# Kernel tuning notes

Hardware: AMD Instinct MI355X
Metric: run time of the kernel (lower is better)

## Reference

```python
import jax, jax.numpy as jnp
import numpy as np

V, E, H, B, T, O = 50000, 300, 512, 32, 256, 10


def setup_inputs() -> dict:
    key = jax.random.key(0)
    ks = jax.random.split(key, 12)
    sc = 1.0 / np.sqrt(H)  # torch LSTM init scale
    rn = lambda k, shape, s: (jax.random.normal(k, shape, jnp.float32) * s)
    return {
        "tokens": jax.random.randint(ks[0], (B, T), 0, V),
        "embed_table": rn(ks[1], (V, E), 0.1),
        "W_ih_f": rn(ks[2], (4 * H, E), sc),
        "W_hh_f": rn(ks[3], (4 * H, H), sc),
        "b_ih_f": rn(ks[4], (4 * H,), sc),
        "b_hh_f": rn(ks[5], (4 * H,), sc),
        "W_ih_b": rn(ks[6], (4 * H, E), sc),
        "W_hh_b": rn(ks[7], (4 * H, H), sc),
        "b_ih_b": rn(ks[8], (4 * H,), sc),
        "b_hh_b": rn(ks[9], (4 * H,), sc),
        "W_out": rn(ks[10], (O, 2 * H), 1.0 / np.sqrt(2 * H)),
        "b_out": rn(ks[11], (O,), 0.01),
    }


def _lstm_dir(x_tbe, W_ih, W_hh, b_ih, b_hh, reverse):
    """One LSTM direction. x_tbe: [T,B,E]. Returns hidden seq [T,B,H]."""
    Hd = W_hh.shape[1]
    # precompute input contribution for all timesteps: [T,B,4H]
    xg = jnp.einsum('tbe,ge->tbg', x_tbe, W_ih) + b_ih + b_hh

    def step(carry, xt):
        h, c = carry
        gates = xt + h @ W_hh.T                    # [B,4H]
        i, f, g, o = jnp.split(gates, 4, axis=-1)  # torch gate order i,f,g,o
        c = jax.nn.sigmoid(f) * c + jax.nn.sigmoid(i) * jnp.tanh(g)
        h = jax.nn.sigmoid(o) * jnp.tanh(c)
        return (h, c), h

    h0 = jnp.zeros((x_tbe.shape[1], Hd), x_tbe.dtype)
    _, hs = jax.lax.scan(step, (h0, h0), xg, reverse=reverse)
    return hs


def reference(tokens, embed_table, W_ih_f, W_hh_f, b_ih_f, b_hh_f,
              W_ih_b, W_hh_b, b_ih_b, b_hh_b, W_out, b_out):
    x = embed_table[tokens]          # [B,T,E] embedding lookup (dropout_e=0 in eval)
    x = x.transpose(1, 0, 2)         # [T,B,E] time-major, as in the torch module
    hf = _lstm_dir(x, W_ih_f, W_hh_f, b_ih_f, b_hh_f, reverse=False)
    hb = _lstm_dir(x, W_ih_b, W_hh_b, b_ih_b, b_hh_b, reverse=True)
    rnn_out = jnp.concatenate([hf, hb], axis=-1)   # [T,B,2H]
    # relu then max-pool over the full time axis (kernel = seq_len)
    pooled = jnp.max(jax.nn.relu(rnn_out), axis=0)  # [B,2H]
    logits = pooled @ W_out.T + b_out               # [B,O]
    return logits, rnn_out
```

## Files before the change

### kernel.cpp

```cpp
#include <hip/hip_runtime.h>
#include <hip/hip_bf16.h>

#define B_ 32
#define T_ 256
#define E_ 300
#define EP_ 320
#define H_ 512
#define O_ 10
#define TEAM 32
#define THR 512
#define HPB 16
#define NBLK 512

typedef __attribute__((ext_vector_type(8))) short bf16x8;
typedef __attribute__((ext_vector_type(4))) float f32x4;

__device__ __forceinline__ float bf2f(unsigned short u) {
  unsigned v = ((unsigned)u) << 16; float f; __builtin_memcpy(&f, &v, 4); return f;
}
__device__ __forceinline__ short f2bf(float x) {
  unsigned u; __builtin_memcpy(&u, &x, 4);
  unsigned r = u + 0x7fffu + ((u >> 16) & 1u);
  return (short)(r >> 16);
}

__global__ __launch_bounds__(256) void xprep_k(
    const int* __restrict__ tokens, const float* __restrict__ embed,
    unsigned short* __restrict__ xb)
{
  const int t = blockIdx.x;
  __shared__ int tok_s[B_];
  const int tid = threadIdx.x;
  if (tid < B_) tok_s[tid] = tokens[tid * T_ + t];
  __syncthreads();
  const size_t plane = (size_t)T_ * B_ * EP_;
  unsigned short* hi = xb;
  unsigned short* lo = xb + plane;
  for (int i = tid; i < B_ * E_; i += 256) {
    const int b = i / E_, e = i - b * E_;
    const float v = embed[(size_t)tok_s[b] * E_ + e];
    const short h = f2bf(v);
    const short l = f2bf(v - bf2f((unsigned short)h));
    const size_t o = ((size_t)t * B_ + b) * EP_ + e;
    hi[o] = (unsigned short)h; lo[o] = (unsigned short)l;
  }
  for (int i = tid; i < B_ * (EP_ - E_); i += 256) {
    const int b = i / (EP_ - E_), e = E_ + (i - b * (EP_ - E_));
    const size_t o = ((size_t)t * B_ + b) * EP_ + e;
    hi[o] = 0; lo[o] = 0;
  }
}

__global__ __launch_bounds__(320) void wprep_k(
    const float* __restrict__ Wf, const float* __restrict__ Wb,
    unsigned short* __restrict__ wp)
{
  const int row = blockIdx.x;
  const int dir = blockIdx.y;
  const int e   = threadIdx.x;
  const float* __restrict__ W = dir ? Wb : Wf;
  short h = 0, l = 0;
  if (e < E_) {
    const float v = W[(size_t)row * E_ + e];
    h = f2bf(v);
    l = f2bf(v - bf2f((unsigned short)h));
  }
  const size_t hiB = ((size_t)(dir * 2 + 0)) * 2048 * EP_;
  const size_t loB = ((size_t)(dir * 2 + 1)) * 2048 * EP_;
  wp[hiB + (size_t)row * EP_ + e] = (unsigned short)h;
  wp[loB + (size_t)row * EP_ + e] = (unsigned short)l;
}

__global__ __launch_bounds__(256) void xg_mfma_k(
    const unsigned short* __restrict__ wp,
    const unsigned short* __restrict__ xb,
    const float* __restrict__ bif, const float* __restrict__ bhf,
    const float* __restrict__ bib, const float* __restrict__ bhb,
    __hip_bfloat16* __restrict__ xg)
{
  const int rt  = blockIdx.x;
  const int t   = blockIdx.y;
  const int dir = blockIdx.z;
  const int tid = threadIdx.x;
  const int l = tid & 63, w = tid >> 6;
  const int m = l & 15, q = l >> 4;
  const int rowb = rt * 64 + w * 16;

  const float* __restrict__ bi = dir ? bib : bif;
  const float* __restrict__ bh = dir ? bhb : bhf;

  bf16x8 ahi[10], alo[10];
  {
    const unsigned short* whi =
        wp + ((size_t)(dir * 2 + 0) * 2048 + rowb + m) * EP_ + q * 8;
    const unsigned short* wlo =
        wp + ((size_t)(dir * 2 + 1) * 2048 + rowb + m) * EP_ + q * 8;
    #pragma unroll
    for (int kt = 0; kt < 10; ++kt) {
      ahi[kt] = *(const bf16x8*)(whi + kt * 32);
      alo[kt] = *(const bf16x8*)(wlo + kt * 32);
    }
  }

  const size_t plane = (size_t)T_ * B_ * EP_;
  const unsigned short* xh0 = xb + ((size_t)t * B_ + m     ) * EP_ + q * 8;
  const unsigned short* xh1 = xb + ((size_t)t * B_ + m + 16) * EP_ + q * 8;

  f32x4 acc0 = {0.f, 0.f, 0.f, 0.f}, acc1 = {0.f, 0.f, 0.f, 0.f};
  #pragma unroll
  for (int kt = 0; kt < 10; ++kt) {
    bf16x8 b0h = *(const bf16x8*)(xh0 + kt * 32);
    bf16x8 b0l = *(const bf16x8*)(xh0 + plane + kt * 32);
    bf16x8 b1h = *(const bf16x8*)(xh1 + kt * 32);
    bf16x8 b1l = *(const bf16x8*)(xh1 + plane + kt * 32);
    acc0 = __builtin_amdgcn_mfma_f32_16x16x32_bf16(ahi[kt], b0h, acc0, 0, 0, 0);
    acc0 = __builtin_amdgcn_mfma_f32_16x16x32_bf16(alo[kt], b0h, acc0, 0, 0, 0);
    acc0 = __builtin_amdgcn_mfma_f32_16x16x32_bf16(ahi[kt], b0l, acc0, 0, 0, 0);
    acc1 = __builtin_amdgcn_mfma_f32_16x16x32_bf16(ahi[kt], b1h, acc1, 0, 0, 0);
    acc1 = __builtin_amdgcn_mfma_f32_16x16x32_bf16(alo[kt], b1h, acc1, 0, 0, 0);
    acc1 = __builtin_amdgcn_mfma_f32_16x16x32_bf16(ahi[kt], b1l, acc1, 0, 0, 0);
  }

  const int r4 = rowb + q * 4;
  const float4 bi4 = *(const float4*)(bi + r4);
  const float4 bh4 = *(const float4*)(bh + r4);
  const float bias0 = bi4.x + bh4.x, bias1 = bi4.y + bh4.y;
  const float bias2 = bi4.z + bh4.z, bias3 = bi4.w + bh4.w;
  unsigned short* og =
      (unsigned short*)xg + ((size_t)(dir * T_ + t) * 2048 + r4) * B_;
  og[0 * B_ + m]      = (unsigned short)f2bf(acc0[0] + bias0);
  og[1 * B_ + m]      = (unsigned short)f2bf(acc0[1] + bias1);
  og[2 * B_ + m]      = (unsigned short)f2bf(acc0[2] + bias2);
  og[3 * B_ + m]      = (unsigned short)f2bf(acc0[3] + bias3);
  og[0 * B_ + m + 16] = (unsigned short)f2bf(acc1[0] + bias0);
  og[1 * B_ + m + 16] = (unsigned short)f2bf(acc1[1] + bias1);
  og[2 * B_ + m + 16] = (unsigned short)f2bf(acc1[2] + bias2);
  og[3 * B_ + m + 16] = (unsigned short)f2bf(acc1[3] + bias3);
}

__device__ __forceinline__ float sigm(float x)    { return 1.f / (1.f + __expf(-x)); }
__device__ __forceinline__ float tanhfast(float x){ return 1.f - 2.f / (__expf(2.f * x) + 1.f); }

__global__ __launch_bounds__(THR) void lstm_rec_k(
    const __hip_bfloat16* __restrict__ xg,
    const float* __restrict__ Whf, const float* __restrict__ Whb,
    unsigned short* __restrict__ ht,
    float* __restrict__ pooled,
    unsigned int* __restrict__ tags, unsigned int* __restrict__ elect)
{
  unsigned xcd;
  asm volatile("s_getreg_b32 %0, hwreg(HW_REG_XCC_ID)" : "=s"(xcd));
  xcd &= 7u;

  __shared__ unsigned rank_s;
  if (threadIdx.x == 0)
    rank_s = __hip_atomic_fetch_add(&elect[xcd], 1u, __ATOMIC_RELAXED,
                                    __HIP_MEMORY_SCOPE_AGENT);
  __syncthreads();
  const unsigned rank = rank_s;
  if (xcd > 1u || rank >= TEAM) return;
  const int dir = (int)xcd;

  const float* __restrict__ Wh = dir ? Whb : Whf;
  const int hs  = (int)rank * HPB;
  const int tid = threadIdx.x;
  const int l   = tid & 63;
  const int wid = tid >> 6;
  const int g   = wid & 3;
  const int kh  = wid >> 2;
  const int hh  = tid & 15, bb = tid >> 4;

  extern __shared__ char lds[];
  float* gp = (float*)(lds + 65536);

  bf16x8 ahi[8], alo[8];
  {
    const int m = l & 15, q = l >> 4;
    const float* wrow = Wh + (size_t)(g * H_ + hs + m) * H_ + kh * 256 + q * 8;
    #pragma unroll
    for (int kt = 0; kt < 8; ++kt) {
      const float* wp = wrow + kt * 32;
      #pragma unroll
      for (int j = 0; j < 8; ++j) {
        const float w = wp[j];
        const short hi = f2bf(w);
        ahi[kt][j] = hi;
        alo[kt][j] = f2bf(w - bf2f((unsigned short)hi));
      }
    }
  }

  const unsigned short* __restrict__ xgu = (const unsigned short*)xg;
  const size_t xco = ((size_t)hs + hh) * B_ + bb;
  unsigned int* __restrict__ mytags = tags + dir * 32;

  float c_st = 0.f, pm = 0.f;

  for (int s = 0; s < T_; ++s) {
    if (s > 0) {
      if (tid < 64) {
        unsigned v = 0xFFFFFFFFu;
        const unsigned int* tp = mytags + (tid & 31);
        int it = 0;
        do {
          if (tid < 32) {
            if (it < 64) {
              asm volatile("global_load_dword %0, %1, off sc0 nt\n\ts_waitcnt vmcnt(0)"
                           : "=v"(v) : "v"(tp) : "memory");
            } else {
              v = __hip_atomic_load(tp, __ATOMIC_RELAXED, __HIP_MEMORY_SCOPE_AGENT);
            }
          }
          ++it;
        } while (__ballot(v < (unsigned)s) != 0ull && it < (1 << 22));
      }
      __syncthreads();
    }

    const int tt = dir ? (T_ - 1 - s) : s;
    const size_t xb = (size_t)(dir * T_ + tt) * 2048 * B_;
    float x0 = bf2f(__builtin_nontemporal_load(xgu + xb + 0 * H_ * B_ + xco));
    float x1 = bf2f(__builtin_nontemporal_load(xgu + xb + 1 * H_ * B_ + xco));
    float x2 = bf2f(__builtin_nontemporal_load(xgu + xb + 2 * H_ * B_ + xco));
    float x3 = bf2f(__builtin_nontemporal_load(xgu + xb + 3 * H_ * B_ + xco));

    if (s > 0) {
      {
        const float4* src = (const float4*)(ht + (size_t)(dir * T_ + (s - 1)) * 32768);
        #pragma unroll
        for (int ii = 0; ii < 8; ++ii) {
          const int i = tid + ii * THR;
          const float4 v4 = src[i];
          const int rk = i >> 7;
          const int f  = i & 127;
          const int pl = f >> 6;
          const int j  = f & 63;
          const int b  = j >> 1;
          const int h0 = (j & 1) * 8;
          const int dst = pl * 32768 +
              ((b * 1024 + (rk * HPB + h0) * 2) ^ ((b & 7) << 4));
          *(float4*)(lds + dst) = v4;
        }
      }
      __syncthreads();
      f32x4 acc0 = {0.f, 0.f, 0.f, 0.f}, acc1 = {0.f, 0.f, 0.f, 0.f};
      {
        const int n0 = l & 15;
        const int swz = (n0 & 7) << 4;
        const int kb = kh * 512 + (l >> 4) * 16;
        #pragma unroll
        for (int kt = 0; kt < 8; ++kt) {
          const int ko = kb + kt * 64;
          const char* p0 = lds + (((n0      ) * 1024 + ko) ^ swz);
          const char* p1 = lds + (((n0 + 16 ) * 1024 + ko) ^ swz);
          bf16x8 b0h = *(const bf16x8*)(p0);
          bf16x8 b0l = *(const bf16x8*)(p0 + 32768);
          bf16x8 b1h = *(const bf16x8*)(p1);
          bf16x8 b1l = *(const bf16x8*)(p1 + 32768);
          acc0 = __builtin_amdgcn_mfma_f32_16x16x32_bf16(ahi[kt], b0h, acc0, 0, 0, 0);
          acc0 = __builtin_amdgcn_mfma_f32_16x16x32_bf16(alo[kt], b0h, acc0, 0, 0, 0);
          acc0 = __builtin_amdgcn_mfma_f32_16x16x32_bf16(ahi[kt], b0l, acc0, 0, 0, 0);
          acc1 = __builtin_amdgcn_mfma_f32_16x16x32_bf16(ahi[kt], b1h, acc1, 0, 0, 0);
          acc1 = __builtin_amdgcn_mfma_f32_16x16x32_bf16(alo[kt], b1h, acc1, 0, 0, 0);
          acc1 = __builtin_amdgcn_mfma_f32_16x16x32_bf16(ahi[kt], b1l, acc1, 0, 0, 0);
        }
      }
      {
        const int slot = (kh * 4 + g) * 32;
        const int rowb = (l >> 4) * 4;
        #pragma unroll
        for (int r = 0; r < 4; ++r) {
          gp[(slot + (l & 15)     ) * 17 + rowb + r] = acc0[r];
          gp[(slot + 16 + (l & 15)) * 17 + rowb + r] = acc1[r];
        }
      }
      __syncthreads();
    }

    float Gi = x0, Gf = x1, Gg = x2, Go = x3;
    if (s > 0) {
      Gi += gp[(0 * 32 + bb) * 17 + hh] + gp[(4 * 32 + bb) * 17 + hh];
      Gf += gp[(1 * 32 + bb) * 17 + hh] + gp[(5 * 32 + bb) * 17 + hh];
      Gg += gp[(2 * 32 + bb) * 17 + hh] + gp[(6 * 32 + bb) * 17 + hh];
      Go += gp[(3 * 32 + bb) * 17 + hh] + gp[(7 * 32 + bb) * 17 + hh];
    }
    c_st = sigm(Gf) * c_st + sigm(Gi) * tanhfast(Gg);
    const float h = sigm(Go) * tanhfast(c_st);
    pm = fmaxf(pm, h);
    {
      const short hi = f2bf(h);
      const short lo = f2bf(h - bf2f((unsigned short)hi));
      unsigned short* region =
          ht + (size_t)(dir * T_ + s) * 32768 + (size_t)rank * 1024;
      region[tid]       = (unsigned short)hi;
      region[512 + tid] = (unsigned short)lo;
    }
    asm volatile("s_waitcnt vmcnt(0)" ::: "memory");
    __syncthreads();
    if (tid == 0) {
      unsigned int* tp = mytags + rank;
      unsigned val = (unsigned)(s + 1);
      asm volatile("global_store_dword %0, %1, off\n\ts_waitcnt vmcnt(0)"
                   :: "v"(tp), "v"(val) : "memory");
    }
  }
  pooled[(size_t)bb * 1024 + dir * H_ + hs + hh] = pm;
}

__global__ __launch_bounds__(256) void finalize_k(
    const unsigned short* __restrict__ ht, float* __restrict__ rnn)
{
  const int t = blockIdx.x, dir = blockIdx.y;
  const int s = dir ? (T_ - 1 - t) : t;
  const unsigned short* slab = ht + (size_t)(dir * T_ + s) * 32768;
  const int b = threadIdx.x >> 3, c = threadIdx.x & 7;
  float* __restrict__ dst = rnn + ((size_t)t * B_ + b) * 1024 + dir * H_;
  #pragma unroll
  for (int j = 0; j < 16; ++j) {
    const int k0 = c * 64 + j * 4;
    const int rk = k0 >> 4;
    const unsigned short* rg = slab + rk * 1024 + b * HPB + (k0 & 15);
    float4 o;
    o.x = bf2f(rg[0]) + bf2f(rg[512 + 0]);
    o.y = bf2f(rg[1]) + bf2f(rg[512 + 1]);
    o.z = bf2f(rg[2]) + bf2f(rg[512 + 2]);
    o.w = bf2f(rg[3]) + bf2f(rg[512 + 3]);
    *(float4*)(dst + k0) = o;
  }
}

__global__ __launch_bounds__(64) void logits_k(
    const float* __restrict__ pooled, const float* __restrict__ Wout,
    const float* __restrict__ bout, float* __restrict__ out)
{
  const int b = blockIdx.x, lane = threadIdx.x;
  float acc[O_];
  #pragma unroll
  for (int o = 0; o < O_; ++o) acc[o] = 0.f;
  for (int k = lane; k < 2 * H_; k += 64) {
    const float pv = pooled[(size_t)b * 1024 + k];
    #pragma unroll
    for (int o = 0; o < O_; ++o) acc[o] += pv * Wout[(size_t)o * 1024 + k];
  }
  #pragma unroll
  for (int o = 0; o < O_; ++o) {
    float v = acc[o];
    #pragma unroll
    for (int off = 32; off > 0; off >>= 1) v += __shfl_down(v, off);
    if (lane == 0) out[b * O_ + o] = v + bout[o];
  }
}

extern "C" void kernel_launch(void* const* d_in, const int* in_sizes, int n_in,
                              void* d_out, int out_size, void* d_ws, size_t ws_size,
                              hipStream_t stream)
{
  const int*   tokens = (const int*)d_in[0];
  const float* embed  = (const float*)d_in[1];
  const float* Wihf   = (const float*)d_in[2];
  const float* Whhf   = (const float*)d_in[3];
  const float* bihf   = (const float*)d_in[4];
  const float* bhhf   = (const float*)d_in[5];
  const float* Wihb   = (const float*)d_in[6];
  const float* Whhb   = (const float*)d_in[7];
  const float* bihb   = (const float*)d_in[8];
  const float* bhhb   = (const float*)d_in[9];
  const float* Wout   = (const float*)d_in[10];
  const float* bout   = (const float*)d_in[11];
  float* out = (float*)d_out;

  char* ws = (char*)d_ws;
  const size_t XG_BYTES = (size_t)2 * T_ * 2048 * B_ * 2;
  const size_t HT_BYTES = (size_t)2 * T_ * 32768 * 2;
  const size_t PL_BYTES = (size_t)B_ * 1024 * 4;
  const size_t TG_BYTES = 2 * 32 * 4;
  const size_t EL_BYTES = 8 * 4;
  if (ws_size < XG_BYTES + HT_BYTES + PL_BYTES + TG_BYTES + EL_BYTES) return;

  __hip_bfloat16* xg     = (__hip_bfloat16*)ws;
  unsigned short* ht     = (unsigned short*)(ws + XG_BYTES);
  float*          pooled = (float*)(ws + XG_BYTES + HT_BYTES);
  unsigned int*   tags   = (unsigned int*)(ws + XG_BYTES + HT_BYTES + PL_BYTES);
  unsigned int*   elect  = (unsigned int*)(ws + XG_BYTES + HT_BYTES + PL_BYTES + TG_BYTES);

  unsigned short* xb = (unsigned short*)(ws + XG_BYTES);
  unsigned short* wpre = (unsigned short*)(ws + XG_BYTES + (size_t)2 * T_ * B_ * EP_ * 2);

  (void)hipMemsetAsync(tags, 0, TG_BYTES + EL_BYTES, stream);

  xprep_k<<<dim3(T_), 256, 0, stream>>>(tokens, embed, xb);
  wprep_k<<<dim3(2048, 2), 320, 0, stream>>>(Wihf, Wihb, wpre);
  xg_mfma_k<<<dim3(32, T_, 2), 256, 0, stream>>>(wpre, xb, bihf, bhhf, bihb, bhhb, xg);

  const int rec_lds = 82944;
  (void)hipFuncSetAttribute((const void*)lstm_rec_k,
                            hipFuncAttributeMaxDynamicSharedMemorySize, rec_lds);
  lstm_rec_k<<<dim3(NBLK), THR, rec_lds, stream>>>(xg, Whhf, Whhb, ht, pooled,
                                                   tags, elect);

  finalize_k<<<dim3(T_, 2), 256, 0, stream>>>(ht, out + B_ * O_);
  logits_k<<<dim3(B_), 64, 0, stream>>>(pooled, Wout, bout, out);
}
```

Measured before the change: 3.282 ms.

## Halve recurrent team size to 16 blocks per direction, 32 hidden units each

The persistent recurrent kernel now uses 16 cooperating workgroups per direction, each owning 32 hidden units (two M-tiles of MFMA) instead of 32 workgroups with 16 units. Each step's cross-block tag polling and synchronization involve fewer participants, at the cost of doubling per-block MFMA work and register-resident weights. The hidden-state exchange layout, gate staging buffer and finalize indexing are adjusted to match, and LDS grows.

```diff
diff --git a/kernel.cpp b/kernel.cpp
--- a/kernel.cpp
+++ b/kernel.cpp
@@ -7,9 +7,9 @@
 #define EP_ 320
 #define H_ 512
 #define O_ 10
-#define TEAM 32
+#define TEAM 16
 #define THR 512
-#define HPB 16
+#define HPB 32
 #define NBLK 512
 
 typedef __attribute__((ext_vector_type(8))) short bf16x8;
@@ -168,15 +168,17 @@
   const int wid = tid >> 6;
   const int g   = wid & 3;
   const int kh  = wid >> 2;
-  const int hh  = tid & 15, bb = tid >> 4;
+  const int cb0 = tid & 31, ch0 = tid >> 5;
 
   extern __shared__ char lds[];
   float* gp = (float*)(lds + 65536);
 
-  bf16x8 ahi[8], alo[8];
-  {
+  bf16x8 ahi[2][8], alo[2][8];
+  #pragma unroll
+  for (int mt = 0; mt < 2; ++mt) {
     const int m = l & 15, q = l >> 4;
-    const float* wrow = Wh + (size_t)(g * H_ + hs + m) * H_ + kh * 256 + q * 8;
+    const float* wrow =
+        Wh + (size_t)(g * H_ + hs + mt * 16 + m) * H_ + kh * 256 + q * 8;
     #pragma unroll
     for (int kt = 0; kt < 8; ++kt) {
       const float* wp = wrow + kt * 32;
@@ -184,26 +186,27 @@
       for (int j = 0; j < 8; ++j) {
         const float w = wp[j];
         const short hi = f2bf(w);
-        ahi[kt][j] = hi;
-        alo[kt][j] = f2bf(w - bf2f((unsigned short)hi));
+        ahi[mt][kt][j] = hi;
+        alo[mt][kt][j] = f2bf(w - bf2f((unsigned short)hi));
       }
     }
   }
 
   const unsigned short* __restrict__ xgu = (const unsigned short*)xg;
-  const size_t xco = ((size_t)hs + hh) * B_ + bb;
+  const size_t xc0 = ((size_t)hs + ch0) * B_ + cb0;
+  const size_t xc1 = ((size_t)hs + ch0 + 16) * B_ + cb0;
   unsigned int* __restrict__ mytags = tags + dir * 32;
 
-  float c_st = 0.f, pm = 0.f;
+  float c0 = 0.f, c1 = 0.f, pm0 = 0.f, pm1 = 0.f;
 
   for (int s = 0; s < T_; ++s) {
     if (s > 0) {
       if (tid < 64) {
         unsigned v = 0xFFFFFFFFu;
-        const unsigned int* tp = mytags + (tid & 31);
+        const unsigned int* tp = mytags + (tid & 15);
         int it = 0;
         do {
-          if (tid < 32) {
+          if (tid < 16) {
             if (it < 64) {
               asm volatile("global_load_dword %0, %1, off sc0 nt\n\ts_waitcnt vmcnt(0)"
                            : "=v"(v) : "v"(tp) : "memory");
@@ -219,10 +222,14 @@
 
     const int tt = dir ? (T_ - 1 - s) : s;
     const size_t xb = (size_t)(dir * T_ + tt) * 2048 * B_;
-    float x0 = bf2f(__builtin_nontemporal_load(xgu + xb + 0 * H_ * B_ + xco));
-    float x1 = bf2f(__builtin_nontemporal_load(xgu + xb + 1 * H_ * B_ + xco));
-    float x2 = bf2f(__builtin_nontemporal_load(xgu + xb + 2 * H_ * B_ + xco));
-    float x3 = bf2f(__builtin_nontemporal_load(xgu + xb + 3 * H_ * B_ + xco));
+    float x0 = bf2f(__builtin_nontemporal_load(xgu + xb + 0 * H_ * B_ + xc0));
+    float x1 = bf2f(__builtin_nontemporal_load(xgu + xb + 1 * H_ * B_ + xc0));
+    float x2 = bf2f(__builtin_nontemporal_load(xgu + xb + 2 * H_ * B_ + xc0));
+    float x3 = bf2f(__builtin_nontemporal_load(xgu + xb + 3 * H_ * B_ + xc0));
+    float x4 = bf2f(__builtin_nontemporal_load(xgu + xb + 0 * H_ * B_ + xc1));
+    float x5 = bf2f(__builtin_nontemporal_load(xgu + xb + 1 * H_ * B_ + xc1));
+    float x6 = bf2f(__builtin_nontemporal_load(xgu + xb + 2 * H_ * B_ + xc1));
+    float x7 = bf2f(__builtin_nontemporal_load(xgu + xb + 3 * H_ * B_ + xc1));
 
     if (s > 0) {
       {
@@ -231,19 +238,24 @@
         for (int ii = 0; ii < 8; ++ii) {
           const int i = tid + ii * THR;
           const float4 v4 = src[i];
-          const int rk = i >> 7;
-          const int f  = i & 127;
-          const int pl = f >> 6;
-          const int j  = f & 63;
-          const int b  = j >> 1;
-          const int h0 = (j & 1) * 8;
+          const int rk = i >> 8;
+          const int f  = i & 255;
+          const int pl = f >> 7;
+          const int j  = f & 127;
+          const int b  = j >> 2;
+          const int k0 = rk * HPB + (j & 3) * 8;
           const int dst = pl * 32768 +
-              ((b * 1024 + (rk * HPB + h0) * 2) ^ ((b & 7) << 4));
+              ((b * 1024 + k0 * 2) ^ ((b & 7) << 4));
           *(float4*)(lds + dst) = v4;
         }
       }
       __syncthreads();
-      f32x4 acc0 = {0.f, 0.f, 0.f, 0.f}, acc1 = {0.f, 0.f, 0.f, 0.f};
+      f32x4 acc[2][2];
+      #pragma unroll
+      for (int mt = 0; mt < 2; ++mt)
+        #pragma unroll
+        for (int nt = 0; nt < 2; ++nt)
+          acc[mt][nt] = (f32x4){0.f, 0.f, 0.f, 0.f};
       {
         const int n0 = l & 15;
         const int swz = (n0 & 7) << 4;
@@ -257,43 +269,62 @@
           bf16x8 b0l = *(const bf16x8*)(p0 + 32768);
           bf16x8 b1h = *(const bf16x8*)(p1);
           bf16x8 b1l = *(const bf16x8*)(p1 + 32768);
-          acc0 = __builtin_amdgcn_mfma_f32_16x16x32_bf16(ahi[kt], b0h, acc0, 0, 0, 0);
-          acc0 = __builtin_amdgcn_mfma_f32_16x16x32_bf16(alo[kt], b0h, acc0, 0, 0, 0);
-          acc0 = __builtin_amdgcn_mfma_f32_16x16x32_bf16(ahi[kt], b0l, acc0, 0, 0, 0);
-          acc1 = __builtin_amdgcn_mfma_f32_16x16x32_bf16(ahi[kt], b1h, acc1, 0, 0, 0);
-          acc1 = __builtin_amdgcn_mfma_f32_16x16x32_bf16(alo[kt], b1h, acc1, 0, 0, 0);
-          acc1 = __builtin_amdgcn_mfma_f32_16x16x32_bf16(ahi[kt], b1l, acc1, 0, 0, 0);
+          #pragma unroll
+          for (int mt = 0; mt < 2; ++mt) {
+            acc[mt][0] = __builtin_amdgcn_mfma_f32_16x16x32_bf16(ahi[mt][kt], b0h, acc[mt][0], 0, 0, 0);
+            acc[mt][0] = __builtin_amdgcn_mfma_f32_16x16x32_bf16(alo[mt][kt], b0h, acc[mt][0], 0, 0, 0);
+            acc[mt][0] = __builtin_amdgcn_mfma_f32_16x16x32_bf16(ahi[mt][kt], b0l, acc[mt][0], 0, 0, 0);
+            acc[mt][1] = __builtin_amdgcn_mfma_f32_16x16x32_bf16(ahi[mt][kt], b1h, acc[mt][1], 0, 0, 0);
+            acc[mt][1] = __builtin_amdgcn_mfma_f32_16x16x32_bf16(alo[mt][kt], b1h, acc[mt][1], 0, 0, 0);
+            acc[mt][1] = __builtin_amdgcn_mfma_f32_16x16x32_bf16(ahi[mt][kt], b1l, acc[mt][1], 0, 0, 0);
+          }
         }
       }
       {
         const int slot = (kh * 4 + g) * 32;
-        const int rowb = (l >> 4) * 4;
         #pragma unroll
-        for (int r = 0; r < 4; ++r) {
-          gp[(slot + (l & 15)     ) * 17 + rowb + r] = acc0[r];
-          gp[(slot + 16 + (l & 15)) * 17 + rowb + r] = acc1[r];
+        for (int mt = 0; mt < 2; ++mt) {
+          const int rowb = mt * 16 + (l >> 4) * 4;
+          #pragma unroll
+          for (int r = 0; r < 4; ++r) {
+            gp[(slot + (l & 15)     ) * 33 + rowb + r] = acc[mt][0][r];
+            gp[(slot + 16 + (l & 15)) * 33 + rowb + r] = acc[mt][1][r];
+          }
         }
       }
       __syncthreads();
     }
 
-    float Gi = x0, Gf = x1, Gg = x2, Go = x3;
+    float Gi0 = x0, Gf0 = x1, Gg0 = x2, Go0 = x3;
+    float Gi1 = x4, Gf1 = x5, Gg1 = x6, Go1 = x7;
     if (s > 0) {
-      Gi += gp[(0 * 32 + bb) * 17 + hh] + gp[(4 * 32 + bb) * 17 + hh];
-      Gf += gp[(1 * 32 + bb) * 17 + hh] + gp[(5 * 32 + bb) * 17 + hh];
-      Gg += gp[(2 * 32 + bb) * 17 + hh] + gp[(6 * 32 + bb) * 17 + hh];
-      Go += gp[(3 * 32 + bb) * 17 + hh] + gp[(7 * 32 + bb) * 17 + hh];
-    }
-    c_st = sigm(Gf) * c_st + sigm(Gi) * tanhfast(Gg);
-    const float h = sigm(Go) * tanhfast(c_st);
-    pm = fmaxf(pm, h);
+      const int r0 = ch0, r1 = ch0 + 16;
+      Gi0 += gp[(0 * 32 + cb0) * 33 + r0] + gp[(4 * 32 + cb0) * 33 + r0];
+      Gf0 += gp[(1 * 32 + cb0) * 33 + r0] + gp[(5 * 32 + cb0) * 33 + r0];
+      Gg0 += gp[(2 * 32 + cb0) * 33 + r0] + gp[(6 * 32 + cb0) * 33 + r0];
+      Go0 += gp[(3 * 32 + cb0) * 33 + r0] + gp[(7 * 32 + cb0) * 33 + r0];
+      Gi1 += gp[(0 * 32 + cb0) * 33 + r1] + gp[(4 * 32 + cb0) * 33 + r1];
+      Gf1 += gp[(1 * 32 + cb0) * 33 + r1] + gp[(5 * 32 + cb0) * 33 + r1];
+      Gg1 += gp[(2 * 32 + cb0) * 33 + r1] + gp[(6 * 32 + cb0) * 33 + r1];
+      Go1 += gp[(3 * 32 + cb0) * 33 + r1] + gp[(7 * 32 + cb0) * 33 + r1];
+    }
+    c0 = sigm(Gf0) * c0 + sigm(Gi0) * tanhfast(Gg0);
+    const float h0v = sigm(Go0) * tanhfast(c0);
+    pm0 = fmaxf(pm0, h0v);
+    c1 = sigm(Gf1) * c1 + sigm(Gi1) * tanhfast(Gg1);
+    const float h1v = sigm(Go1) * tanhfast(c1);
+    pm1 = fmaxf(pm1, h1v);
     {
-      const short hi = f2bf(h);
-      const short lo = f2bf(h - bf2f((unsigned short)hi));
       unsigned short* region =
-          ht + (size_t)(dir * T_ + s) * 32768 + (size_t)rank * 1024;
-      region[tid]       = (unsigned short)hi;
-      region[512 + tid] = (unsigned short)lo;
+          ht + (size_t)(dir * T_ + s) * 32768 + (size_t)rank * 2048;
+      const int e0 = cb0 * HPB + ch0;
+      const int e1 = e0 + 16;
+      const short hi0 = f2bf(h0v);
+      const short hi1 = f2bf(h1v);
+      region[e0]        = (unsigned short)hi0;
+      region[1024 + e0] = (unsigned short)f2bf(h0v - bf2f((unsigned short)hi0));
+      region[e1]        = (unsigned short)hi1;
+      region[1024 + e1] = (unsigned short)f2bf(h1v - bf2f((unsigned short)hi1));
     }
     asm volatile("s_waitcnt vmcnt(0)" ::: "memory");
     __syncthreads();
@@ -304,7 +335,8 @@
                    :: "v"(tp), "v"(val) : "memory");
     }
   }
-  pooled[(size_t)bb * 1024 + dir * H_ + hs + hh] = pm;
+  pooled[(size_t)cb0 * 1024 + dir * H_ + hs + ch0]      = pm0;
+  pooled[(size_t)cb0 * 1024 + dir * H_ + hs + ch0 + 16] = pm1;
 }
 
 __global__ __launch_bounds__(256) void finalize_k(
@@ -318,13 +350,14 @@
   #pragma unroll
   for (int j = 0; j < 16; ++j) {
     const int k0 = c * 64 + j * 4;
-    const int rk = k0 >> 4;
-    const unsigned short* rg = slab + rk * 1024 + b * HPB + (k0 & 15);
+    const int rk = k0 >> 5;
+    const int hl = k0 & 31;
+    const unsigned short* rg = slab + rk * 2048 + b * HPB + hl;
     float4 o;
-    o.x = bf2f(rg[0]) + bf2f(rg[512 + 0]);
-    o.y = bf2f(rg[1]) + bf2f(rg[512 + 1]);
-    o.z = bf2f(rg[2]) + bf2f(rg[512 + 2]);
-    o.w = bf2f(rg[3]) + bf2f(rg[512 + 3]);
+    o.x = bf2f(rg[0]) + bf2f(rg[1024 + 0]);
+    o.y = bf2f(rg[1]) + bf2f(rg[1024 + 1]);
+    o.z = bf2f(rg[2]) + bf2f(rg[1024 + 2]);
+    o.w = bf2f(rg[3]) + bf2f(rg[1024 + 3]);
     *(float4*)(dst + k0) = o;
   }
 }
@@ -392,7 +425,7 @@
   wprep_k<<<dim3(2048, 2), 320, 0, stream>>>(Wihf, Wihb, wpre);
   xg_mfma_k<<<dim3(32, T_, 2), 256, 0, stream>>>(wpre, xb, bihf, bhhf, bihb, bhhb, xg);
 
-  const int rec_lds = 82944;
+  const int rec_lds = 99328;
   (void)hipFuncSetAttribute((const void*)lstm_rec_k,
                             hipFuncAttributeMaxDynamicSharedMemorySize, rec_lds);
   lstm_rec_k<<<dim3(NBLK), THR, rec_lds, stream>>>(xg, Whhf, Whhb, ht, pooled,
```

Result: no change. 3.340 ms (+1.8%).

## Fuse input-projection GEMM into recurrent LSTM kernel, overlapping it with spin-wait

Applied to the files above, without the earlier changes.

Drops the separate xg_mfma_k kernel and the bf16 xg buffer. Each recurrent block now keeps its slice of W_ih as hi/lo bf16 registers and computes the input projection for the current timestep with MFMA before waiting on the inter-block tag barrier. This overlaps that work with the synchronisation latency and removes a kernel launch plus the xg write and read. In exchange it adds register pressure and puts extra MFMA and global loads inside the serial per-step loop.

```diff
diff --git a/kernel.cpp b/kernel.cpp
--- a/kernel.cpp
+++ b/kernel.cpp
@@ -71,79 +71,15 @@
   wp[loB + (size_t)row * EP_ + e] = (unsigned short)l;
 }
 
-__global__ __launch_bounds__(256) void xg_mfma_k(
+__device__ __forceinline__ float sigm(float x)    { return 1.f / (1.f + __expf(-x)); }
+__device__ __forceinline__ float tanhfast(float x){ return 1.f - 2.f / (__expf(2.f * x) + 1.f); }
+
+__global__ __launch_bounds__(THR) void lstm_rec_k(
+    const unsigned short* __restrict__ xbuf,
     const unsigned short* __restrict__ wp,
-    const unsigned short* __restrict__ xb,
+    const float* __restrict__ Whf, const float* __restrict__ Whb,
     const float* __restrict__ bif, const float* __restrict__ bhf,
     const float* __restrict__ bib, const float* __restrict__ bhb,
-    __hip_bfloat16* __restrict__ xg)
-{
-  const int rt  = blockIdx.x;
-  const int t   = blockIdx.y;
-  const int dir = blockIdx.z;
-  const int tid = threadIdx.x;
-  const int l = tid & 63, w = tid >> 6;
-  const int m = l & 15, q = l >> 4;
-  const int rowb = rt * 64 + w * 16;
-
-  const float* __restrict__ bi = dir ? bib : bif;
-  const float* __restrict__ bh = dir ? bhb : bhf;
-
-  bf16x8 ahi[10], alo[10];
-  {
-    const unsigned short* whi =
-        wp + ((size_t)(dir * 2 + 0) * 2048 + rowb + m) * EP_ + q * 8;
-    const unsigned short* wlo =
-        wp + ((size_t)(dir * 2 + 1) * 2048 + rowb + m) * EP_ + q * 8;
-    #pragma unroll
-    for (int kt = 0; kt < 10; ++kt) {
-      ahi[kt] = *(const bf16x8*)(whi + kt * 32);
-      alo[kt] = *(const bf16x8*)(wlo + kt * 32);
-    }
-  }
-
-  const size_t plane = (size_t)T_ * B_ * EP_;
-  const unsigned short* xh0 = xb + ((size_t)t * B_ + m     ) * EP_ + q * 8;
-  const unsigned short* xh1 = xb + ((size_t)t * B_ + m + 16) * EP_ + q * 8;
-
-  f32x4 acc0 = {0.f, 0.f, 0.f, 0.f}, acc1 = {0.f, 0.f, 0.f, 0.f};
-  #pragma unroll
-  for (int kt = 0; kt < 10; ++kt) {
-    bf16x8 b0h = *(const bf16x8*)(xh0 + kt * 32);
-    bf16x8 b0l = *(const bf16x8*)(xh0 + plane + kt * 32);
-    bf16x8 b1h = *(const bf16x8*)(xh1 + kt * 32);
-    bf16x8 b1l = *(const bf16x8*)(xh1 + plane + kt * 32);
-    acc0 = __builtin_amdgcn_mfma_f32_16x16x32_bf16(ahi[kt], b0h, acc0, 0, 0, 0);
-    acc0 = __builtin_amdgcn_mfma_f32_16x16x32_bf16(alo[kt], b0h, acc0, 0, 0, 0);
-    acc0 = __builtin_amdgcn_mfma_f32_16x16x32_bf16(ahi[kt], b0l, acc0, 0, 0, 0);
-    acc1 = __builtin_amdgcn_mfma_f32_16x16x32_bf16(ahi[kt], b1h, acc1, 0, 0, 0);
-    acc1 = __builtin_amdgcn_mfma_f32_16x16x32_bf16(alo[kt], b1h, acc1, 0, 0, 0);
-    acc1 = __builtin_amdgcn_mfma_f32_16x16x32_bf16(ahi[kt], b1l, acc1, 0, 0, 0);
-  }
-
-  const int r4 = rowb + q * 4;
-  const float4 bi4 = *(const float4*)(bi + r4);
-  const float4 bh4 = *(const float4*)(bh + r4);
-  const float bias0 = bi4.x + bh4.x, bias1 = bi4.y + bh4.y;
-  const float bias2 = bi4.z + bh4.z, bias3 = bi4.w + bh4.w;
-  unsigned short* og =
-      (unsigned short*)xg + ((size_t)(dir * T_ + t) * 2048 + r4) * B_;
-  og[0 * B_ + m]      = (unsigned short)f2bf(acc0[0] + bias0);
-  og[1 * B_ + m]      = (unsigned short)f2bf(acc0[1] + bias1);
-  og[2 * B_ + m]      = (unsigned short)f2bf(acc0[2] + bias2);
-  og[3 * B_ + m]      = (unsigned short)f2bf(acc0[3] + bias3);
-  og[0 * B_ + m + 16] = (unsigned short)f2bf(acc1[0] + bias0);
-  og[1 * B_ + m + 16] = (unsigned short)f2bf(acc1[1] + bias1);
-  og[2 * B_ + m + 16] = (unsigned short)f2bf(acc1[2] + bias2);
-  og[3 * B_ + m + 16] = (unsigned short)f2bf(acc1[3] + bias3);
-}
-
-__device__ __forceinline__ float sigm(float x)    { return 1.f / (1.f + __expf(-x)); }
-__device__ __forceinline__ float tanhfast(float x){ return 1.f - 2.f / (__expf(2.f * x) + 1.f); }
-
-__global__ __launch_bounds__(THR) void lstm_rec_k(
-    const __hip_bfloat16* __restrict__ xg,
-    const float* __restrict__ Whf, const float* __restrict__ Whb,
     unsigned short* __restrict__ ht,
     float* __restrict__ pooled,
     unsigned int* __restrict__ tags, unsigned int* __restrict__ elect)
@@ -162,6 +98,8 @@
   const int dir = (int)xcd;
 
   const float* __restrict__ Wh = dir ? Whb : Whf;
+  const float* __restrict__ bi = dir ? bib : bif;
+  const float* __restrict__ bh = dir ? bhb : bhf;
   const int hs  = (int)rank * HPB;
   const int tid = threadIdx.x;
   const int l   = tid & 63;
@@ -179,24 +117,63 @@
     const float* wrow = Wh + (size_t)(g * H_ + hs + m) * H_ + kh * 256 + q * 8;
     #pragma unroll
     for (int kt = 0; kt < 8; ++kt) {
-      const float* wp = wrow + kt * 32;
+      const float* wpr = wrow + kt * 32;
       #pragma unroll
       for (int j = 0; j < 8; ++j) {
-        const float w = wp[j];
+        const float w = wpr[j];
         const short hi = f2bf(w);
         ahi[kt][j] = hi;
         alo[kt][j] = f2bf(w - bf2f((unsigned short)hi));
       }
     }
   }
-
-  const unsigned short* __restrict__ xgu = (const unsigned short*)xg;
-  const size_t xco = ((size_t)hs + hh) * B_ + bb;
+  bf16x8 xhi[5], xlo[5];
+  {
+    const int m = l & 15, q = l >> 4;
+    const unsigned short* whi =
+        wp + ((size_t)(dir * 2 + 0) * 2048 + g * H_ + hs + m) * EP_ + kh * 160 + q * 8;
+    const unsigned short* wlo =
+        wp + ((size_t)(dir * 2 + 1) * 2048 + g * H_ + hs + m) * EP_ + kh * 160 + q * 8;
+    #pragma unroll
+    for (int kt = 0; kt < 5; ++kt) {
+      xhi[kt] = *(const bf16x8*)(whi + kt * 32);
+      xlo[kt] = *(const bf16x8*)(wlo + kt * 32);
+    }
+  }
+  float bsum[4];
+  #pragma unroll
+  for (int gg2 = 0; gg2 < 4; ++gg2)
+    bsum[gg2] = bi[gg2 * H_ + hs + hh] + bh[gg2 * H_ + hs + hh];
+
+  const size_t xplane = (size_t)T_ * B_ * EP_;
   unsigned int* __restrict__ mytags = tags + dir * 32;
 
   float c_st = 0.f, pm = 0.f;
 
   for (int s = 0; s < T_; ++s) {
+    const int tt = dir ? (T_ - 1 - s) : s;
+    f32x4 acc0 = {0.f, 0.f, 0.f, 0.f}, acc1 = {0.f, 0.f, 0.f, 0.f};
+    {
+      const int n0 = l & 15, q = l >> 4;
+      const unsigned short* x0p =
+          xbuf + ((size_t)tt * B_ + n0     ) * EP_ + kh * 160 + q * 8;
+      const unsigned short* x1p =
+          xbuf + ((size_t)tt * B_ + n0 + 16) * EP_ + kh * 160 + q * 8;
+      #pragma unroll
+      for (int kt = 0; kt < 5; ++kt) {
+        bf16x8 b0h = *(const bf16x8*)(x0p + kt * 32);
+        bf16x8 b0l = *(const bf16x8*)(x0p + xplane + kt * 32);
+        bf16x8 b1h = *(const bf16x8*)(x1p + kt * 32);
+        bf16x8 b1l = *(const bf16x8*)(x1p + xplane + kt * 32);
+        acc0 = __builtin_amdgcn_mfma_f32_16x16x32_bf16(xhi[kt], b0h, acc0, 0, 0, 0);
+        acc0 = __builtin_amdgcn_mfma_f32_16x16x32_bf16(xlo[kt], b0h, acc0, 0, 0, 0);
+        acc0 = __builtin_amdgcn_mfma_f32_16x16x32_bf16(xhi[kt], b0l, acc0, 0, 0, 0);
+        acc1 = __builtin_amdgcn_mfma_f32_16x16x32_bf16(xhi[kt], b1h, acc1, 0, 0, 0);
+        acc1 = __builtin_amdgcn_mfma_f32_16x16x32_bf16(xlo[kt], b1h, acc1, 0, 0, 0);
+        acc1 = __builtin_amdgcn_mfma_f32_16x16x32_bf16(xhi[kt], b1l, acc1, 0, 0, 0);
+      }
+    }
+
     if (s > 0) {
       if (tid < 64) {
         unsigned v = 0xFFFFFFFFu;
@@ -215,16 +192,6 @@
         } while (__ballot(v < (unsigned)s) != 0ull && it < (1 << 22));
       }
       __syncthreads();
-    }
-
-    const int tt = dir ? (T_ - 1 - s) : s;
-    const size_t xb = (size_t)(dir * T_ + tt) * 2048 * B_;
-    float x0 = bf2f(__builtin_nontemporal_load(xgu + xb + 0 * H_ * B_ + xco));
-    float x1 = bf2f(__builtin_nontemporal_load(xgu + xb + 1 * H_ * B_ + xco));
-    float x2 = bf2f(__builtin_nontemporal_load(xgu + xb + 2 * H_ * B_ + xco));
-    float x3 = bf2f(__builtin_nontemporal_load(xgu + xb + 3 * H_ * B_ + xco));
-
-    if (s > 0) {
       {
         const float4* src = (const float4*)(ht + (size_t)(dir * T_ + (s - 1)) * 32768);
         #pragma unroll
@@ -243,7 +210,6 @@
         }
       }
       __syncthreads();
-      f32x4 acc0 = {0.f, 0.f, 0.f, 0.f}, acc1 = {0.f, 0.f, 0.f, 0.f};
       {
         const int n0 = l & 15;
         const int swz = (n0 & 7) << 4;
@@ -265,25 +231,22 @@
           acc1 = __builtin_amdgcn_mfma_f32_16x16x32_bf16(ahi[kt], b1l, acc1, 0, 0, 0);
         }
       }
-      {
-        const int slot = (kh * 4 + g) * 32;
-        const int rowb = (l >> 4) * 4;
-        #pragma unroll
-        for (int r = 0; r < 4; ++r) {
-          gp[(slot + (l & 15)     ) * 17 + rowb + r] = acc0[r];
-          gp[(slot + 16 + (l & 15)) * 17 + rowb + r] = acc1[r];
-        }
-      }
-      __syncthreads();
-    }
-
-    float Gi = x0, Gf = x1, Gg = x2, Go = x3;
-    if (s > 0) {
-      Gi += gp[(0 * 32 + bb) * 17 + hh] + gp[(4 * 32 + bb) * 17 + hh];
-      Gf += gp[(1 * 32 + bb) * 17 + hh] + gp[(5 * 32 + bb) * 17 + hh];
-      Gg += gp[(2 * 32 + bb) * 17 + hh] + gp[(6 * 32 + bb) * 17 + hh];
-      Go += gp[(3 * 32 + bb) * 17 + hh] + gp[(7 * 32 + bb) * 17 + hh];
-    }
+    }
+    {
+      const int slot = (kh * 4 + g) * 32;
+      const int rowb = (l >> 4) * 4;
+      #pragma unroll
+      for (int r = 0; r < 4; ++r) {
+        gp[(slot + (l & 15)     ) * 17 + rowb + r] = acc0[r];
+        gp[(slot + 16 + (l & 15)) * 17 + rowb + r] = acc1[r];
+      }
+    }
+    __syncthreads();
+
+    const float Gi = gp[(0 * 32 + bb) * 17 + hh] + gp[(4 * 32 + bb) * 17 + hh] + bsum[0];
+    const float Gf = gp[(1 * 32 + bb) * 17 + hh] + gp[(5 * 32 + bb) * 17 + hh] + bsum[1];
+    const float Gg = gp[(2 * 32 + bb) * 17 + hh] + gp[(6 * 32 + bb) * 17 + hh] + bsum[2];
+    const float Go = gp[(3 * 32 + bb) * 17 + hh] + gp[(7 * 32 + bb) * 17 + hh] + bsum[3];
     c_st = sigm(Gf) * c_st + sigm(Gi) * tanhfast(Gg);
     const float h = sigm(Go) * tanhfast(c_st);
     pm = fmaxf(pm, h);
@@ -370,33 +333,32 @@
   float* out = (float*)d_out;
 
   char* ws = (char*)d_ws;
-  const size_t XG_BYTES = (size_t)2 * T_ * 2048 * B_ * 2;
+  const size_t XB_BYTES = (size_t)2 * T_ * B_ * EP_ * 2;
+  const size_t WP_BYTES = (size_t)2 * 2 * 2048 * EP_ * 2;
   const size_t HT_BYTES = (size_t)2 * T_ * 32768 * 2;
   const size_t PL_BYTES = (size_t)B_ * 1024 * 4;
   const size_t TG_BYTES = 2 * 32 * 4;
   const size_t EL_BYTES = 8 * 4;
-  if (ws_size < XG_BYTES + HT_BYTES + PL_BYTES + TG_BYTES + EL_BYTES) return;
-
-  __hip_bfloat16* xg     = (__hip_bfloat16*)ws;
-  unsigned short* ht     = (unsigned short*)(ws + XG_BYTES);
-  float*          pooled = (float*)(ws + XG_BYTES + HT_BYTES);
-  unsigned int*   tags   = (unsigned int*)(ws + XG_BYTES + HT_BYTES + PL_BYTES);
-  unsigned int*   elect  = (unsigned int*)(ws + XG_BYTES + HT_BYTES + PL_BYTES + TG_BYTES);
-
-  unsigned short* xb = (unsigned short*)(ws + XG_BYTES);
-  unsigned short* wpre = (unsigned short*)(ws + XG_BYTES + (size_t)2 * T_ * B_ * EP_ * 2);
+  if (ws_size < XB_BYTES + WP_BYTES + HT_BYTES + PL_BYTES + TG_BYTES + EL_BYTES)
+    return;
+
+  unsigned short* xb     = (unsigned short*)ws;
+  unsigned short* wpre   = (unsigned short*)(ws + XB_BYTES);
+  unsigned short* ht     = (unsigned short*)(ws + XB_BYTES + WP_BYTES);
+  float*          pooled = (float*)(ws + XB_BYTES + WP_BYTES + HT_BYTES);
+  unsigned int*   tags   = (unsigned int*)(ws + XB_BYTES + WP_BYTES + HT_BYTES + PL_BYTES);
+  unsigned int*   elect  = (unsigned int*)(ws + XB_BYTES + WP_BYTES + HT_BYTES + PL_BYTES + TG_BYTES);
 
   (void)hipMemsetAsync(tags, 0, TG_BYTES + EL_BYTES, stream);
 
   xprep_k<<<dim3(T_), 256, 0, stream>>>(tokens, embed, xb);
   wprep_k<<<dim3(2048, 2), 320, 0, stream>>>(Wihf, Wihb, wpre);
-  xg_mfma_k<<<dim3(32, T_, 2), 256, 0, stream>>>(wpre, xb, bihf, bhhf, bihb, bhhb, xg);
 
   const int rec_lds = 82944;
   (void)hipFuncSetAttribute((const void*)lstm_rec_k,
                             hipFuncAttributeMaxDynamicSharedMemorySize, rec_lds);
-  lstm_rec_k<<<dim3(NBLK), THR, rec_lds, stream>>>(xg, Whhf, Whhb, ht, pooled,
-                                                   tags, elect);
+  lstm_rec_k<<<dim3(NBLK), THR, rec_lds, stream>>>(
+      xb, wpre, Whhf, Whhb, bihf, bhhf, bihb, bhhb, ht, pooled, tags, elect);
 
   finalize_k<<<dim3(T_, 2), 256, 0, stream>>>(ht, out + B_ * O_);
   logits_k<<<dim3(B_), 64, 0, stream>>>(pooled, Wout, bout, out);
```

Result: slower. 3.814 ms (+16.2%).
